# Kernel tuning notes

Hardware: AMD Instinct MI355X
Metric: run time of the kernel (lower is better)

Reference implementation:

```python
import jax, jax.numpy as jnp
import numpy as np

D = 512
H = 8
DH = D // H
EPS = 1e-5


def _layernorm(x, g, b):
    mu = jnp.mean(x, axis=-1, keepdims=True)
    var = jnp.mean((x - mu) ** 2, axis=-1, keepdims=True)
    return (x - mu) * jax.lax.rsqrt(var + EPS) * g + b


def setup_inputs() -> dict:
    key = jax.random.key(0)
    ks = jax.random.split(key, 10)
    B, S = 4, 2048
    s = 1.0 / np.sqrt(D)
    return {
        "x": jax.random.normal(ks[0], (B, S, D), dtype=jnp.float32),
        "Wq": jax.random.normal(ks[1], (D, D), dtype=jnp.float32) * s,
        "Wk": jax.random.normal(ks[2], (D, D), dtype=jnp.float32) * s,
        "Wv": jax.random.normal(ks[3], (D, D), dtype=jnp.float32) * s,
        "Wo": jax.random.normal(ks[4], (D, D), dtype=jnp.float32) * s,
        "W1": jax.random.normal(ks[5], (4 * D, D), dtype=jnp.float32) * s,
        "b1": jnp.zeros((4 * D,), dtype=jnp.float32),
        "W2": jax.random.normal(ks[6], (D, 4 * D), dtype=jnp.float32) * (1.0 / np.sqrt(4 * D)),
        "b2": jnp.zeros((D,), dtype=jnp.float32),
        "g1": jnp.ones((D,), dtype=jnp.float32),
        "bb1": jnp.zeros((D,), dtype=jnp.float32),
        "g2": jnp.ones((D,), dtype=jnp.float32),
        "bb2": jnp.zeros((D,), dtype=jnp.float32),
    }


def reference(x, Wq, Wk, Wv, Wo, W1, b1, W2, b2, g1, bb1, g2, bb2):
    B, S, _ = x.shape
    # projections (torch Linear: y = x @ W.T), split heads: chunk(-1) == reshape to [B,S,H,DH]
    q = (x @ Wq.T).reshape(B, S, H, DH).transpose(0, 2, 1, 3)  # [B,H,S,DH]
    k = (x @ Wk.T).reshape(B, S, H, DH).transpose(0, 2, 1, 3)
    v = (x @ Wv.T).reshape(B, S, H, DH).transpose(0, 2, 1, 3)
    scores = jnp.einsum("bhsd,bhtd->bhst", q, k) / np.sqrt(DH)  # [B,H,S,S]
    attn = jax.nn.softmax(scores, axis=-1)
    ctx = jnp.einsum("bhst,bhtd->bhsd", attn, v)  # [B,H,S,DH]
    ctx = ctx.transpose(0, 2, 1, 3).reshape(B, S, D)
    h = _layernorm(x + ctx @ Wo.T, g1, bb1)
    mlp = jax.nn.relu(h @ W1.T + b1) @ W2.T + b2
    return _layernorm(h + mlp, g2, bb2)
```

## Files before the change

kernel.cpp:

```cpp
#include <hip/hip_runtime.h>
#include <hip/hip_bf16.h>
#include <cstdint>
#include <cstddef>

typedef short bf16x8 __attribute__((ext_vector_type(8)));
typedef float floatx4 __attribute__((ext_vector_type(4)));
typedef unsigned short u16;

constexpr int B = 4, S = 2048, D = 512, H = 8, DH = 64;
constexpr int M_ROWS = B * S;
constexpr int D4 = 4 * D;
constexpr float QSCALE = 0.18033688011112042f;

__device__ __forceinline__ u16 f2b(float f) {
  unsigned u = __builtin_bit_cast(unsigned, f);
  u += 0x7fff + ((u >> 16) & 1);
  return (u16)(u >> 16);
}

__device__ __forceinline__ bf16x8 ldfrag(const u16* p) {
  return *reinterpret_cast<const bf16x8*>(p);
}

__device__ __forceinline__ floatx4 mfma16(bf16x8 a, bf16x8 b, floatx4 c) {
  return __builtin_amdgcn_mfma_f32_16x16x32_bf16(a, b, c, 0, 0, 0);
}

__device__ __forceinline__ ushort4 f2b4(float4 v) {
  ushort4 r;
  r.x = f2b(v.x); r.y = f2b(v.y); r.z = f2b(v.z); r.w = f2b(v.w);
  return r;
}

__device__ __forceinline__ void gld16(const u16* g, u16* l) {
  __builtin_amdgcn_global_load_lds(
      (const __attribute__((address_space(1))) void*)g,
      (__attribute__((address_space(3))) void*)l, 16, 0, 0);
}

__global__ void cast4_kernel(const float4* __restrict__ in, ushort4* __restrict__ out, int n4) {
  int i = blockIdx.x * blockDim.x + threadIdx.x;
  if (i < n4) out[i] = f2b4(in[i]);
}

__global__ void cast_w_kernel(const float4* __restrict__ w1, const float4* __restrict__ w2,
                              const float4* __restrict__ wq, const float4* __restrict__ wk,
                              const float4* __restrict__ wv, const float4* __restrict__ wo,
                              ushort4* __restrict__ w1b, ushort4* __restrict__ w2b,
                              ushort4* __restrict__ wqb, ushort4* __restrict__ wkb,
                              ushort4* __restrict__ wvb, ushort4* __restrict__ wob) {
  int i = blockIdx.x * blockDim.x + threadIdx.x;
  constexpr int N1 = (D4 * D) / 4;
  constexpr int NS = (D * D) / 4;
  if (i < N1) { w1b[i] = f2b4(w1[i]); return; }
  i -= N1;
  if (i < N1) { w2b[i] = f2b4(w2[i]); return; }
  i -= N1;
  const int sel = i >> 16, off = i & (NS - 1);
  const float4* src = sel == 0 ? wq : sel == 1 ? wk : sel == 2 ? wv : wo;
  ushort4* dst = sel == 0 ? wqb : sel == 1 ? wkb : sel == 2 ? wvb : wob;
  dst[off] = f2b4(src[off]);
}

template <int EPI>
__global__ __launch_bounds__(256) void gemm_bt(
    const u16* __restrict__ A, const u16* __restrict__ W,
    const float* __restrict__ bias, void* __restrict__ out0, void* __restrict__ out1,
    int M, int N, int K, int klen) {
  __shared__ __align__(16) u16 As[2 * 128 * 32];
  __shared__ __align__(16) u16 Bs[2 * 128 * 32];
  const int wave = threadIdx.x >> 6, lane = threadIdx.x & 63;
  const int quad = lane >> 4, l16 = lane & 15;
  const int rowB = blockIdx.y * 128, colB = blockIdx.x * 128;
  const int rowW = (wave >> 1) * 64, colW = (wave & 1) * 64;
  const int koff = blockIdx.z * klen;
  void* out = blockIdx.z ? out1 : out0;

  floatx4 acc[4][4];
#pragma unroll
  for (int i = 0; i < 4; i++)
#pragma unroll
    for (int j = 0; j < 4; j++) acc[i][j] = (floatx4){0.f,0.f,0.f,0.f};

  const u16* gA = A + (size_t)(rowB + wave * 32 + (lane >> 2)) * K + koff + (lane & 3) * 8;
  const u16* gB = W + (size_t)(colB + wave * 32 + (lane >> 2)) * K + koff + (lane & 3) * 8;
  u16* lA = As + (wave * 32) * 32;
  u16* lB = Bs + (wave * 32) * 32;

  for (int kc = 0; kc < klen; kc += 64) {
#pragma unroll
    for (int kk = 0; kk < 2; kk++)
#pragma unroll
      for (int rr = 0; rr < 2; rr++) {
        gld16(gA + (size_t)rr * 16 * K + kc + kk * 32, lA + kk * 4096 + rr * 16 * 32);
        gld16(gB + (size_t)rr * 16 * K + kc + kk * 32, lB + kk * 4096 + rr * 16 * 32);
      }
    __syncthreads();

#pragma unroll
    for (int kk = 0; kk < 2; kk++) {
      bf16x8 a[4], b[4];
#pragma unroll
      for (int i = 0; i < 4; i++)
        a[i] = ldfrag(&As[kk * 4096 + (rowW + i * 16 + l16) * 32 + quad * 8]);
#pragma unroll
      for (int j = 0; j < 4; j++)
        b[j] = ldfrag(&Bs[kk * 4096 + (colW + j * 16 + l16) * 32 + quad * 8]);
#pragma unroll
      for (int i = 0; i < 4; i++)
#pragma unroll
        for (int j = 0; j < 4; j++) acc[i][j] = mfma16(a[i], b[j], acc[i][j]);
    }
    __syncthreads();
  }

#pragma unroll
  for (int i = 0; i < 4; i++) {
#pragma unroll
    for (int j = 0; j < 4; j++) {
      const int gn = colB + colW + j * 16 + l16;
      const float bv = (EPI == 1) ? bias[gn] : 0.f;
#pragma unroll
      for (int r = 0; r < 4; r++) {
        const int gm = rowB + rowW + i * 16 + quad * 4 + r;
        float v = acc[i][j][r] + bv;
        if (EPI == 0) {
          ((float*)out)[(size_t)gm * N + gn] = v;
        } else {
          v = v > 0.f ? v : 0.f;
          ((u16*)out)[(size_t)gm * N + gn] = f2b(v);
        }
      }
    }
  }
}

__global__ __launch_bounds__(256) void qkv_gemm(
    const u16* __restrict__ xb,
    const u16* __restrict__ wq, const u16* __restrict__ wk, const u16* __restrict__ wv,
    u16* __restrict__ q, u16* __restrict__ k, u16* __restrict__ vT) {
  __shared__ __align__(16) u16 As[2 * 128 * 32];
  __shared__ __align__(16) u16 Bs[2 * 128 * 32];
  const int which = blockIdx.z;
  const u16* __restrict__ W = which == 0 ? wq : (which == 1 ? wk : wv);
  const int wave = threadIdx.x >> 6, lane = threadIdx.x & 63;
  const int quad = lane >> 4, l16 = lane & 15;
  const int rowB = blockIdx.y * 128, colB = blockIdx.x * 128;
  const int rowW = (wave >> 1) * 64, colW = (wave & 1) * 64;

  floatx4 acc[4][4];
#pragma unroll
  for (int i = 0; i < 4; i++)
#pragma unroll
    for (int j = 0; j < 4; j++) acc[i][j] = (floatx4){0.f,0.f,0.f,0.f};

  const u16* gA = xb + (size_t)(rowB + wave * 32 + (lane >> 2)) * D + (lane & 3) * 8;
  const u16* gB = W + (size_t)(colB + wave * 32 + (lane >> 2)) * D + (lane & 3) * 8;
  u16* lA = As + (wave * 32) * 32;
  u16* lB = Bs + (wave * 32) * 32;

  for (int kc = 0; kc < D; kc += 64) {
#pragma unroll
    for (int kk = 0; kk < 2; kk++)
#pragma unroll
      for (int rr = 0; rr < 2; rr++) {
        gld16(gA + (size_t)rr * 16 * D + kc + kk * 32, lA + kk * 4096 + rr * 16 * 32);
        gld16(gB + (size_t)rr * 16 * D + kc + kk * 32, lB + kk * 4096 + rr * 16 * 32);
      }
    __syncthreads();

#pragma unroll
    for (int kk = 0; kk < 2; kk++) {
      bf16x8 a[4], b[4];
#pragma unroll
      for (int i = 0; i < 4; i++)
        a[i] = ldfrag(&As[kk * 4096 + (rowW + i * 16 + l16) * 32 + quad * 8]);
#pragma unroll
      for (int j = 0; j < 4; j++)
        b[j] = ldfrag(&Bs[kk * 4096 + (colW + j * 16 + l16) * 32 + quad * 8]);
#pragma unroll
      for (int i = 0; i < 4; i++)
#pragma unroll
        for (int j = 0; j < 4; j++) acc[i][j] = mfma16(a[i], b[j], acc[i][j]);
    }
    __syncthreads();
  }

  const float oscale = (which == 0) ? QSCALE : 1.0f;
  u16* dst01 = which == 0 ? q : k;
#pragma unroll
  for (int i = 0; i < 4; i++) {
#pragma unroll
    for (int j = 0; j < 4; j++) {
      const int gn = colB + colW + j * 16 + l16;
      const int h = gn >> 6, dh = gn & 63;
#pragma unroll
      for (int r = 0; r < 4; r++) {
        const int gm = rowB + rowW + i * 16 + quad * 4 + r;
        const int bb = gm >> 11, s = gm & 2047;
        const u16 val = f2b(acc[i][j][r] * oscale);
        if (which < 2) {
          dst01[((((size_t)bb * H + h) * S) + s) * DH + dh] = val;
        } else {
          vT[((((size_t)bb * H + h) * DH) + dh) * S + s] = val;
        }
      }
    }
  }
}

constexpr int PSTRIDE = 72;

__global__ __launch_bounds__(512) void attn_kernel(
    const u16* __restrict__ q, const u16* __restrict__ k,
    const u16* __restrict__ vT, u16* __restrict__ ctxb) {
  __shared__ __align__(16) u16 plds[8][64 * PSTRIDE];
  const int wave = threadIdx.x >> 6, lane = threadIdx.x & 63;
  const int quad = lane >> 4, l16 = lane & 15;
  const int pair = wave >> 1, khalf = wave & 1;
  const int blk = (blockIdx.x & 7) * 32 + (blockIdx.x >> 3);
  const int w = blk * 4 + pair;
  const int bh = w >> 5;
  const int qt = w & 31;
  const int bb = bh >> 3, h = bh & 7;

  const u16* qp = q + ((size_t)bh * S + qt * 64 + l16) * DH + quad * 8;
  bf16x8 qf[4][2];
#pragma unroll
  for (int t = 0; t < 4; t++) {
    qf[t][0] = ldfrag(qp + (size_t)t * 16 * DH);
    qf[t][1] = ldfrag(qp + (size_t)t * 16 * DH + 32);
  }
  const u16* kbase = k + (size_t)bh * S * DH + (size_t)(khalf * 1024 + l16) * DH + quad * 8;
  const u16* vbase = vT + (size_t)bh * DH * S + (size_t)l16 * S + khalf * 1024 + quad * 8;

  floatx4 o[4][4];
#pragma unroll
  for (int t = 0; t < 4; t++)
#pragma unroll
    for (int c = 0; c < 4; c++) o[t][c] = (floatx4){0.f,0.f,0.f,0.f};
  float lacc[4][4];
#pragma unroll
  for (int t = 0; t < 4; t++)
#pragma unroll
    for (int r = 0; r < 4; r++) lacc[t][r] = 0.f;

  u16* myp = plds[wave];
  u16* wp = myp + (quad * 4) * PSTRIDE + l16;
  const u16* rp = myp + l16 * PSTRIDE + quad * 8;

  for (int kt = 0; kt < S / 2; kt += 64) {
    const u16* kp = kbase + (size_t)kt * DH;
    bf16x8 kf[8];
#pragma unroll
    for (int i = 0; i < 4; i++) {
      kf[2 * i]     = ldfrag(kp + (size_t)i * 16 * DH);
      kf[2 * i + 1] = ldfrag(kp + (size_t)i * 16 * DH + 32);
    }
    const u16* vp = vbase + kt;
    bf16x8 vf[8];
#pragma unroll
    for (int c = 0; c < 4; c++) {
      vf[2 * c]     = ldfrag(vp + (size_t)c * 16 * S);
      vf[2 * c + 1] = ldfrag(vp + (size_t)c * 16 * S + 32);
    }

    floatx4 sc[4][4];
#pragma unroll
    for (int t = 0; t < 4; t++)
#pragma unroll
      for (int i = 0; i < 4; i++) {
        floatx4 z = (floatx4){0.f,0.f,0.f,0.f};
        z = mfma16(qf[t][0], kf[2 * i], z);
        z = mfma16(qf[t][1], kf[2 * i + 1], z);
        sc[t][i] = z;
      }

#pragma unroll
    for (int t = 0; t < 4; t++)
#pragma unroll
      for (int r = 0; r < 4; r++) {
        float acc = 0.f;
#pragma unroll
        for (int i = 0; i < 4; i++) {
          const float p = __builtin_amdgcn_exp2f(sc[t][i][r]);
          acc += p;
          wp[(t * 16 + r) * PSTRIDE + i * 16] = f2b(p);
        }
        lacc[t][r] += acc;
      }

#pragma unroll
    for (int t = 0; t < 4; t++) {
      const bf16x8 pf0 = *reinterpret_cast<const bf16x8*>(rp + (size_t)t * 16 * PSTRIDE);
      const bf16x8 pf1 = *reinterpret_cast<const bf16x8*>(rp + (size_t)t * 16 * PSTRIDE + 32);
#pragma unroll
      for (int c = 0; c < 4; c++) {
        o[t][c] = mfma16(pf0, vf[2 * c], o[t][c]);
        o[t][c] = mfma16(pf1, vf[2 * c + 1], o[t][c]);
      }
    }
  }

  float lr[4][4];
#pragma unroll
  for (int t = 0; t < 4; t++)
#pragma unroll
    for (int r = 0; r < 4; r++) {
      float l = lacc[t][r];
#pragma unroll
      for (int d = 1; d < 16; d <<= 1) l += __shfl_xor(l, d);
      lr[t][r] = l;
    }

  float* ob = reinterpret_cast<float*>(plds[2 * pair]);
  float* lb = ob + 64 * 64;

  __syncthreads();
  if (khalf == 1) {
#pragma unroll
    for (int t = 0; t < 4; t++)
#pragma unroll
      for (int c = 0; c < 4; c++)
        *reinterpret_cast<floatx4*>(&ob[lane * 64 + (t * 4 + c) * 4]) = o[t][c];
    if (l16 == 0) {
#pragma unroll
      for (int t = 0; t < 4; t++)
#pragma unroll
        for (int r = 0; r < 4; r++) lb[t * 16 + quad * 4 + r] = lr[t][r];
    }
  }
  __syncthreads();
  if (khalf == 0) {
    float inv[4][4];
#pragma unroll
    for (int t = 0; t < 4; t++)
#pragma unroll
      for (int r = 0; r < 4; r++)
        inv[t][r] = 1.0f / (lr[t][r] + lb[t * 16 + quad * 4 + r]);

    const size_t crow_base = ((size_t)bb * S) * D + h * DH;
#pragma unroll
    for (int t = 0; t < 4; t++)
#pragma unroll
      for (int c = 0; c < 4; c++) {
        const floatx4 oo = o[t][c] +
            *reinterpret_cast<const floatx4*>(&ob[lane * 64 + (t * 4 + c) * 4]);
        const int dh = c * 16 + l16;
#pragma unroll
        for (int r = 0; r < 4; r++) {
          const int s = qt * 64 + t * 16 + quad * 4 + r;
          ctxb[crow_base + (size_t)s * D + dh] = f2b(oo[r] * inv[t][r]);
        }
      }
  }
}

template <bool BF16OUT, bool PB>
__global__ __launch_bounds__(256) void ln_kernel(
    const float* __restrict__ resid, const float* __restrict__ ya,
    const float* __restrict__ yb, const float* __restrict__ pb,
    const float* __restrict__ g, const float* __restrict__ bvec,
    float* __restrict__ outF, u16* __restrict__ outB) {
  const int wave = threadIdx.x >> 6, lane = threadIdx.x & 63;
  const int row = blockIdx.x * 4 + wave;
  const float* rp = resid + (size_t)row * D + lane * 8;
  const float* ap = ya + (size_t)row * D + lane * 8;
  const float* bp = yb + (size_t)row * D + lane * 8;
  float v[8];
  const float4 r0 = *(const float4*)rp, r1 = *(const float4*)(rp + 4);
  const float4 a0 = *(const float4*)ap, a1 = *(const float4*)(ap + 4);
  const float4 b0 = *(const float4*)bp, b1 = *(const float4*)(bp + 4);
  v[0] = r0.x + a0.x + b0.x; v[1] = r0.y + a0.y + b0.y;
  v[2] = r0.z + a0.z + b0.z; v[3] = r0.w + a0.w + b0.w;
  v[4] = r1.x + a1.x + b1.x; v[5] = r1.y + a1.y + b1.y;
  v[6] = r1.z + a1.z + b1.z; v[7] = r1.w + a1.w + b1.w;
  if (PB) {
    const float4 p0 = *(const float4*)(pb + lane * 8);
    const float4 p1 = *(const float4*)(pb + lane * 8 + 4);
    v[0] += p0.x; v[1] += p0.y; v[2] += p0.z; v[3] += p0.w;
    v[4] += p1.x; v[5] += p1.y; v[6] += p1.z; v[7] += p1.w;
  }
  float sum = 0.f;
#pragma unroll
  for (int i = 0; i < 8; i++) sum += v[i];
#pragma unroll
  for (int d = 1; d < 64; d <<= 1) sum += __shfl_xor(sum, d);
  const float mu = sum * (1.f / D);
  float vs = 0.f;
#pragma unroll
  for (int i = 0; i < 8; i++) { const float t = v[i] - mu; vs += t * t; }
#pragma unroll
  for (int d = 1; d < 64; d <<= 1) vs += __shfl_xor(vs, d);
  const float rstd = rsqrtf(vs * (1.f / D) + 1e-5f);
#pragma unroll
  for (int i = 0; i < 8; i++) {
    const int col = lane * 8 + i;
    const float o = (v[i] - mu) * rstd * g[col] + bvec[col];
    outF[(size_t)row * D + col] = o;
    if (BF16OUT) outB[(size_t)row * D + col] = f2b(o);
  }
}

constexpr size_t OFF_XB  = 0;
constexpr size_t OFF_WQB = 8u << 20;
constexpr size_t OFF_WKB = OFF_WQB + (512u << 10);
constexpr size_t OFF_WVB = OFF_WKB + (512u << 10);
constexpr size_t OFF_WOB = OFF_WVB + (512u << 10);
constexpr size_t OFF_W1B = 10u << 20;
constexpr size_t OFF_W2B = 12u << 20;
constexpr size_t OFF_Q   = 14u << 20;
constexpr size_t OFF_K   = 22u << 20;
constexpr size_t OFF_VT  = 30u << 20;
constexpr size_t OFF_CTX = 38u << 20;
constexpr size_t OFF_Y   = 46u << 20;
constexpr size_t OFF_H   = 62u << 20;
constexpr size_t OFF_HB  = 78u << 20;
constexpr size_t OFF_M1B = 86u << 20;

extern "C" void kernel_launch(void* const* d_in, const int* in_sizes, int n_in,
                              void* d_out, int out_size, void* d_ws, size_t ws_size,
                              hipStream_t stream) {
  const float* x  = (const float*)d_in[0];
  const float* Wq = (const float*)d_in[1];
  const float* Wk = (const float*)d_in[2];
  const float* Wv = (const float*)d_in[3];
  const float* Wo = (const float*)d_in[4];
  const float* W1 = (const float*)d_in[5];
  const float* b1 = (const float*)d_in[6];
  const float* W2 = (const float*)d_in[7];
  const float* b2 = (const float*)d_in[8];
  const float* g1 = (const float*)d_in[9];
  const float* bb1 = (const float*)d_in[10];
  const float* g2 = (const float*)d_in[11];
  const float* bb2 = (const float*)d_in[12];

  char* ws = (char*)d_ws;
  u16* xb  = (u16*)(ws + OFF_XB);
  u16* wqb = (u16*)(ws + OFF_WQB);
  u16* wkb = (u16*)(ws + OFF_WKB);
  u16* wvb = (u16*)(ws + OFF_WVB);
  u16* wob = (u16*)(ws + OFF_WOB);
  u16* w1b = (u16*)(ws + OFF_W1B);
  u16* w2b = (u16*)(ws + OFF_W2B);
  u16* qb  = (u16*)(ws + OFF_Q);
  u16* kb  = (u16*)(ws + OFF_K);
  u16* vtb = (u16*)(ws + OFF_VT);
  u16* ctxb = (u16*)(ws + OFF_CTX);
  float* y0 = (float*)(ws + OFF_Y);
  float* y1 = (float*)(ws + OFF_Q);
  float* hf = (float*)(ws + OFF_H);
  u16* hb  = (u16*)(ws + OFF_HB);
  u16* m1b = (u16*)(ws + OFF_M1B);

  cast4_kernel<<<(M_ROWS * D / 4 + 255) / 256, 256, 0, stream>>>(
      (const float4*)x, (ushort4*)xb, M_ROWS * D / 4);
  {
    const int n4 = (D4 * D) / 4 * 2 + (D * D) / 4 * 4;
    cast_w_kernel<<<(n4 + 255) / 256, 256, 0, stream>>>(
        (const float4*)W1, (const float4*)W2, (const float4*)Wq, (const float4*)Wk,
        (const float4*)Wv, (const float4*)Wo,
        (ushort4*)w1b, (ushort4*)w2b, (ushort4*)wqb, (ushort4*)wkb,
        (ushort4*)wvb, (ushort4*)wob);
  }

  qkv_gemm<<<dim3(D / 128, M_ROWS / 128, 3), 256, 0, stream>>>(xb, wqb, wkb, wvb, qb, kb, vtb);

  attn_kernel<<<B * H * S / 64 / 4, 512, 0, stream>>>(qb, kb, vtb, ctxb);

  gemm_bt<0><<<dim3(D / 128, M_ROWS / 128, 2), 256, 0, stream>>>(
      ctxb, wob, nullptr, y0, y1, M_ROWS, D, D, D / 2);

  ln_kernel<true, false><<<M_ROWS / 4, 256, 0, stream>>>(
      x, y0, y1, nullptr, g1, bb1, hf, hb);

  gemm_bt<1><<<dim3(D4 / 128, M_ROWS / 128, 1), 256, 0, stream>>>(
      hb, w1b, b1, m1b, nullptr, M_ROWS, D4, D, D);

  gemm_bt<0><<<dim3(D / 128, M_ROWS / 128, 2), 256, 0, stream>>>(
      m1b, w2b, nullptr, y0, y1, M_ROWS, D, D4, D4 / 2);

  ln_kernel<false, true><<<M_ROWS / 4, 256, 0, stream>>>(
      hf, y0, y1, b2, g2, bb2, (float*)d_out, nullptr);
}
```

Measured before the change: 304.1 us.

## Stage K/V tiles in double-buffered LDS shared across attention waves

Restructures the attention kernel so that each block of 4 waves, which all work on the same head, cooperatively loads K and V tiles into double-buffered shared memory with async global-to-LDS loads. Each wave now covers the full key range instead of splitting keys between wave pairs, which removes the cross-wave O/l reduction through LDS. The score MFMA is transposed so each lane holds 4 consecutive keys for a query, allowing packed P stores and a cheaper row-sum reduction. The trade-offs are a block-wide barrier on every tile, half as many threads per block, and a longer serial key loop per wave.

```diff
diff --git a/kernel.cpp b/kernel.cpp
--- a/kernel.cpp
+++ b/kernel.cpp
@@ -209,19 +209,19 @@
   }
 }
 
-constexpr int PSTRIDE = 72;
-
-__global__ __launch_bounds__(512) void attn_kernel(
+constexpr int PST = 72;
+
+__global__ __launch_bounds__(256, 1) void attn_kernel(
     const u16* __restrict__ q, const u16* __restrict__ k,
     const u16* __restrict__ vT, u16* __restrict__ ctxb) {
-  __shared__ __align__(16) u16 plds[8][64 * PSTRIDE];
+  __shared__ __align__(16) u16 kvlds[2][2][2][64 * 32];
+  __shared__ __align__(16) u16 plds[4][64 * PST];
+  __shared__ float lb[4][64];
   const int wave = threadIdx.x >> 6, lane = threadIdx.x & 63;
   const int quad = lane >> 4, l16 = lane & 15;
-  const int pair = wave >> 1, khalf = wave & 1;
   const int blk = (blockIdx.x & 7) * 32 + (blockIdx.x >> 3);
-  const int w = blk * 4 + pair;
-  const int bh = w >> 5;
-  const int qt = w & 31;
+  const int w = blk * 4 + wave;
+  const int bh = w >> 5, qt = w & 31;
   const int bb = bh >> 3, h = bh & 7;
 
   const u16* qp = q + ((size_t)bh * S + qt * 64 + l16) * DH + quad * 8;
@@ -231,69 +231,79 @@
     qf[t][0] = ldfrag(qp + (size_t)t * 16 * DH);
     qf[t][1] = ldfrag(qp + (size_t)t * 16 * DH + 32);
   }
-  const u16* kbase = k + (size_t)bh * S * DH + (size_t)(khalf * 1024 + l16) * DH + quad * 8;
-  const u16* vbase = vT + (size_t)bh * DH * S + (size_t)l16 * S + khalf * 1024 + quad * 8;
+
+  const int st = threadIdx.x;
+  const int srow = st >> 2, sp = (st & 3) * 8;
+  const u16* kS = k + (size_t)bh * S * DH + (size_t)srow * DH + sp;
+  const u16* vS = vT + (size_t)bh * DH * S + (size_t)srow * S + sp;
 
   floatx4 o[4][4];
 #pragma unroll
   for (int t = 0; t < 4; t++)
 #pragma unroll
     for (int c = 0; c < 4; c++) o[t][c] = (floatx4){0.f,0.f,0.f,0.f};
-  float lacc[4][4];
-#pragma unroll
-  for (int t = 0; t < 4; t++)
-#pragma unroll
-    for (int r = 0; r < 4; r++) lacc[t][r] = 0.f;
+  float lacc[4] = {0.f, 0.f, 0.f, 0.f};
 
   u16* myp = plds[wave];
-  u16* wp = myp + (quad * 4) * PSTRIDE + l16;
-  const u16* rp = myp + l16 * PSTRIDE + quad * 8;
-
-  for (int kt = 0; kt < S / 2; kt += 64) {
-    const u16* kp = kbase + (size_t)kt * DH;
-    bf16x8 kf[8];
+  u16* wpb = myp + l16 * PST + quad * 4;
+  const u16* rpb = myp + l16 * PST + quad * 8;
+
+  {
+    gld16(kS, &kvlds[0][0][0][wave * 512]);
+    gld16(kS + 32, &kvlds[0][0][1][wave * 512]);
+    gld16(vS, &kvlds[0][1][0][wave * 512]);
+    gld16(vS + 32, &kvlds[0][1][1][wave * 512]);
+  }
+
+  int buf = 0;
+  for (int kt = 0; kt < S; kt += 64, buf ^= 1) {
+    __syncthreads();
+
+    bf16x8 kf[8], vf[8];
 #pragma unroll
     for (int i = 0; i < 4; i++) {
-      kf[2 * i]     = ldfrag(kp + (size_t)i * 16 * DH);
-      kf[2 * i + 1] = ldfrag(kp + (size_t)i * 16 * DH + 32);
-    }
-    const u16* vp = vbase + kt;
-    bf16x8 vf[8];
-#pragma unroll
-    for (int c = 0; c < 4; c++) {
-      vf[2 * c]     = ldfrag(vp + (size_t)c * 16 * S);
-      vf[2 * c + 1] = ldfrag(vp + (size_t)c * 16 * S + 32);
-    }
-
-    floatx4 sc[4][4];
-#pragma unroll
-    for (int t = 0; t < 4; t++)
+      kf[2 * i]     = ldfrag(&kvlds[buf][0][0][(i * 16 + l16) * 32 + quad * 8]);
+      kf[2 * i + 1] = ldfrag(&kvlds[buf][0][1][(i * 16 + l16) * 32 + quad * 8]);
+      vf[2 * i]     = ldfrag(&kvlds[buf][1][0][(i * 16 + l16) * 32 + quad * 8]);
+      vf[2 * i + 1] = ldfrag(&kvlds[buf][1][1][(i * 16 + l16) * 32 + quad * 8]);
+    }
+
+    if (kt + 64 < S) {
+      const int nb = buf ^ 1;
+      gld16(kS + (size_t)(kt + 64) * DH, &kvlds[nb][0][0][wave * 512]);
+      gld16(kS + (size_t)(kt + 64) * DH + 32, &kvlds[nb][0][1][wave * 512]);
+      gld16(vS + kt + 64, &kvlds[nb][1][0][wave * 512]);
+      gld16(vS + kt + 96, &kvlds[nb][1][1][wave * 512]);
+    }
+
+#pragma unroll
+    for (int t = 0; t < 4; t++) {
+      floatx4 sc[4];
 #pragma unroll
       for (int i = 0; i < 4; i++) {
         floatx4 z = (floatx4){0.f,0.f,0.f,0.f};
-        z = mfma16(qf[t][0], kf[2 * i], z);
-        z = mfma16(qf[t][1], kf[2 * i + 1], z);
-        sc[t][i] = z;
-      }
-
-#pragma unroll
-    for (int t = 0; t < 4; t++)
-#pragma unroll
-      for (int r = 0; r < 4; r++) {
-        float acc = 0.f;
-#pragma unroll
-        for (int i = 0; i < 4; i++) {
-          const float p = __builtin_amdgcn_exp2f(sc[t][i][r]);
-          acc += p;
-          wp[(t * 16 + r) * PSTRIDE + i * 16] = f2b(p);
-        }
-        lacc[t][r] += acc;
-      }
+        z = mfma16(kf[2 * i], qf[t][0], z);
+        z = mfma16(kf[2 * i + 1], qf[t][1], z);
+        sc[i] = z;
+      }
+      float a = 0.f;
+#pragma unroll
+      for (int i = 0; i < 4; i++) {
+        const float p0 = __builtin_amdgcn_exp2f(sc[i][0]);
+        const float p1 = __builtin_amdgcn_exp2f(sc[i][1]);
+        const float p2 = __builtin_amdgcn_exp2f(sc[i][2]);
+        const float p3 = __builtin_amdgcn_exp2f(sc[i][3]);
+        a += (p0 + p1) + (p2 + p3);
+        ushort4 pk = {f2b(p0), f2b(p1), f2b(p2), f2b(p3)};
+        *reinterpret_cast<ushort4*>(&wpb[t * 16 * PST + i * 16]) = pk;
+      }
+      lacc[t] += a;
+    }
 
 #pragma unroll
     for (int t = 0; t < 4; t++) {
-      const bf16x8 pf0 = *reinterpret_cast<const bf16x8*>(rp + (size_t)t * 16 * PSTRIDE);
-      const bf16x8 pf1 = *reinterpret_cast<const bf16x8*>(rp + (size_t)t * 16 * PSTRIDE + 32);
+      const bf16x8 pf0 = ldfrag(rpb + (size_t)t * 16 * PST);
+      const bf16x8 pf1 = ldfrag(rpb + (size_t)t * 16 * PST + 32);
 #pragma unroll
       for (int c = 0; c < 4; c++) {
         o[t][c] = mfma16(pf0, vf[2 * c], o[t][c]);
@@ -302,58 +312,38 @@
     }
   }
 
-  float lr[4][4];
+  float lt[4];
+#pragma unroll
+  for (int t = 0; t < 4; t++) {
+    float l = lacc[t];
+    l += __shfl_xor(l, 16);
+    l += __shfl_xor(l, 32);
+    lt[t] = l;
+  }
+  if (quad == 0) {
+#pragma unroll
+    for (int t = 0; t < 4; t++) lb[wave][t * 16 + l16] = lt[t];
+  }
+  __builtin_amdgcn_wave_barrier();
+  float inv[4][4];
 #pragma unroll
   for (int t = 0; t < 4; t++)
 #pragma unroll
-    for (int r = 0; r < 4; r++) {
-      float l = lacc[t][r];
-#pragma unroll
-      for (int d = 1; d < 16; d <<= 1) l += __shfl_xor(l, d);
-      lr[t][r] = l;
-    }
-
-  float* ob = reinterpret_cast<float*>(plds[2 * pair]);
-  float* lb = ob + 64 * 64;
-
-  __syncthreads();
-  if (khalf == 1) {
-#pragma unroll
-    for (int t = 0; t < 4; t++)
-#pragma unroll
-      for (int c = 0; c < 4; c++)
-        *reinterpret_cast<floatx4*>(&ob[lane * 64 + (t * 4 + c) * 4]) = o[t][c];
-    if (l16 == 0) {
-#pragma unroll
-      for (int t = 0; t < 4; t++)
-#pragma unroll
-        for (int r = 0; r < 4; r++) lb[t * 16 + quad * 4 + r] = lr[t][r];
-    }
-  }
-  __syncthreads();
-  if (khalf == 0) {
-    float inv[4][4];
-#pragma unroll
-    for (int t = 0; t < 4; t++)
-#pragma unroll
-      for (int r = 0; r < 4; r++)
-        inv[t][r] = 1.0f / (lr[t][r] + lb[t * 16 + quad * 4 + r]);
-
-    const size_t crow_base = ((size_t)bb * S) * D + h * DH;
-#pragma unroll
-    for (int t = 0; t < 4; t++)
-#pragma unroll
-      for (int c = 0; c < 4; c++) {
-        const floatx4 oo = o[t][c] +
-            *reinterpret_cast<const floatx4*>(&ob[lane * 64 + (t * 4 + c) * 4]);
-        const int dh = c * 16 + l16;
-#pragma unroll
-        for (int r = 0; r < 4; r++) {
-          const int s = qt * 64 + t * 16 + quad * 4 + r;
-          ctxb[crow_base + (size_t)s * D + dh] = f2b(oo[r] * inv[t][r]);
-        }
-      }
-  }
+    for (int r = 0; r < 4; r++)
+      inv[t][r] = 1.0f / lb[wave][t * 16 + quad * 4 + r];
+
+  const size_t crow_base = ((size_t)bb * S) * D + h * DH;
+#pragma unroll
+  for (int t = 0; t < 4; t++)
+#pragma unroll
+    for (int c = 0; c < 4; c++) {
+      const int dh = c * 16 + l16;
+#pragma unroll
+      for (int r = 0; r < 4; r++) {
+        const int s = qt * 64 + t * 16 + quad * 4 + r;
+        ctxb[crow_base + (size_t)s * D + dh] = f2b(o[t][c][r] * inv[t][r]);
+      }
+    }
 }
 
 template <bool BF16OUT, bool PB>
@@ -466,7 +456,7 @@
 
   qkv_gemm<<<dim3(D / 128, M_ROWS / 128, 3), 256, 0, stream>>>(xb, wqb, wkb, wvb, qb, kb, vtb);
 
-  attn_kernel<<<B * H * S / 64 / 4, 512, 0, stream>>>(qb, kb, vtb, ctxb);
+  attn_kernel<<<B * H * S / 64 / 4, 256, 0, stream>>>(qb, kb, vtb, ctxb);
 
   gemm_bt<0><<<dim3(D / 128, M_ROWS / 128, 2), 256, 0, stream>>>(
       ctxb, wob, nullptr, y0, y1, M_ROWS, D, D, D / 2);
```

New measurement: 286.0 us. 1.06x faster.
